# Performance work log

Hardware: AMD Instinct MI355X
Metric: run time of the kernel (lower is better)

Reference implementation:

```python
import jax, jax.numpy as jnp
import numpy as np

B, N, HD = 4, 16384, 1024
H, M = 8, 32
D = HD // H  # 128


def setup_inputs() -> dict:
    key = jax.random.key(0)
    ks = jax.random.split(key, 8)
    std = 0.02
    x = jax.random.normal(ks[0], (B, N, HD), dtype=jnp.float32)
    wt_kv_weight = jax.random.normal(ks[1], (2 * HD, HD), dtype=jnp.float32) * std
    wt_kv_bias = jnp.zeros((2 * HD,), dtype=jnp.float32)
    wtq = jax.random.normal(ks[2], (H, M, D), dtype=jnp.float32) * std
    wtq_bias = jnp.zeros((H, M), dtype=jnp.float32)  # registered buffer, zeros
    qkv_proj = jax.random.normal(ks[3], (H, D, 3 * D), dtype=jnp.float32) * std
    out_weight = jax.random.normal(ks[4], (HD, HD), dtype=jnp.float32) * std
    out_bias = jnp.zeros((HD,), dtype=jnp.float32)
    return {
        'x': x,
        'wt_kv_weight': wt_kv_weight,
        'wt_kv_bias': wt_kv_bias,
        'wtq': wtq,
        'wtq_bias': wtq_bias,
        'qkv_proj': qkv_proj,
        'out_weight': out_weight,
        'out_bias': out_bias,
    }


def reference(x, wt_kv_weight, wt_kv_bias, wtq, wtq_bias, qkv_proj, out_weight, out_bias):
    b, n, hd = x.shape
    h, m, d = wtq.shape
    # wt_kv_proj: Linear(hd, 2hd); torch Linear: x @ W.T + b
    kv = x @ wt_kv_weight.T + wt_kv_bias  # [b, n, 2hd]
    xk, xv = jnp.split(kv, 2, axis=-1)
    xk = xk.reshape(b, n, h, d).transpose(0, 2, 1, 3)  # b h n d
    xv = xv.reshape(b, n, h, d).transpose(0, 2, 1, 3)  # b h n d
    # qk_norm=False -> no normalize
    slice_scores = jnp.einsum('hmd,bhnd->bhmn', wtq, xk)
    slice_weights = jax.nn.softmax(slice_scores, axis=-2)  # softmax over slice axis m
    bias = wtq_bias[..., None]  # [h, m, 1]
    slice_token = jnp.einsum('bhmn,bhnd->bhmd', slice_weights, xv)
    slice_norm = jnp.sum(slice_weights, axis=-1, keepdims=True)  # [b,h,m,1]
    slice_token = slice_token / (slice_norm + 1e-5)
    qkv_token = jnp.einsum('bhmd,hde->bhme', slice_token, qkv_proj)  # e = 3d
    q_tok, k_tok, v_tok = jnp.split(qkv_token, 3, axis=-1)
    scale = d ** (-0.5)
    dots = jnp.einsum('bhqd,bhkd->bhqk', q_tok, k_tok) * scale
    attn_weights = jax.nn.softmax(dots, axis=-1)
    out_token = jnp.einsum('bhqk,bhkd->bhqd', attn_weights, v_tok)
    # scatter back via slice weights
    out = jnp.einsum('bhmd,bhmn->bhnd', out_token, slice_weights)
    out = out.transpose(0, 2, 1, 3).reshape(b, n, hd)
    out = out @ out_weight.T + out_bias  # to_out linear (dropout=0)
    temperature = jnp.asarray(1.0, dtype=x.dtype)
    return (out, slice_weights, temperature, bias, attn_weights)
```

## Files before the change

### kernel.cpp

```cpp
#include <hip/hip_runtime.h>
#include <hip/hip_bf16.h>
#include <stdint.h>

#define BB 4
#define NN 16384
#define HDIM 1024
#define HH 8
#define MM 32
#define DD 128

typedef unsigned int u32;
typedef unsigned short u16;
typedef __attribute__((ext_vector_type(8))) short short8;
typedef __attribute__((ext_vector_type(4))) float f32x4;

__device__ __forceinline__ float bf2f(u16 v) {
    union { u32 u; float f; } c; c.u = ((u32)v) << 16; return c.f;
}
__device__ __forceinline__ u16 f2bf(float f) {
    union { float f; u32 u; } c; c.f = f;
    u32 r = c.u + 0x7fffu + ((c.u >> 16) & 1u);
    return (u16)(r >> 16);
}

__device__ __forceinline__ void gload16(const u16* g, u16* l) {
    __builtin_amdgcn_global_load_lds(
        (const __attribute__((address_space(1))) void*)g,
        (__attribute__((address_space(3))) void*)l, 16, 0, 0);
}

#define MFMA16(a, b, c) __builtin_amdgcn_mfma_f32_16x16x32_bf16(a, b, c, 0, 0, 0)

__global__ __launch_bounds__(256) void convert_kernel(const float* __restrict__ x,
                                                      u16* __restrict__ xb, u16* __restrict__ xbT,
                                                      const float* __restrict__ wtq_bias,
                                                      float* __restrict__ out_misc) {
    __shared__ u32 tl[128 * 65];
    const int t = threadIdx.x;
    const int eb = blockIdx.x & 7;
    const int nb = blockIdx.x >> 3;
    const size_t n0 = (size_t)nb * 128;
    const int e0 = eb * 128;

#pragma unroll 4
    for (int i = 0; i < 32; i++) {
        const int idx = t + i * 256;
        const int nl = idx >> 6, e2 = idx & 63;
        const float2 v = *(const float2*)&x[(n0 + nl) * 1024 + e0 + e2 * 2];
        const u32 pk = (u32)f2bf(v.x) | ((u32)f2bf(v.y) << 16);
        ((u32*)xb)[((n0 + nl) * 1024 + e0) / 2 + e2] = pk;
        tl[nl * 65 + e2] = pk;
    }
    __syncthreads();
    const int b = (int)(n0 >> 14);
    const int nloc = (int)(n0 & 16383);
#pragma unroll 4
    for (int i = 0; i < 32; i++) {
        const int idx = t + i * 256;
        const int el = idx >> 6, n2 = idx & 63;
        const u32 w0 = tl[(2 * n2) * 65 + (el >> 1)];
        const u32 w1 = tl[(2 * n2 + 1) * 65 + (el >> 1)];
        const int sh = (el & 1) * 16;
        const u32 o = ((w0 >> sh) & 0xffffu) | (((w1 >> sh) & 0xffffu) << 16);
        ((u32*)xbT)[((size_t)(b * 1024 + e0 + el) * 16384 + nloc + 2 * n2) >> 1] = o;
    }
    if (blockIdx.x == 0) {
        if (t == 0) out_misc[0] = 1.0f;
        if (t < HH * MM) out_misc[1 + t] = wtq_bias[t];
    }
}

__global__ __launch_bounds__(256) void wq_kernel(const float* __restrict__ wtq,
                                                 const float* __restrict__ wkv,
                                                 const float* __restrict__ bkv,
                                                 u16* __restrict__ WQb, float* __restrict__ wqbias,
                                                 u16* __restrict__ wvb) {
    __shared__ float wtql[MM * DD];
    const int ec = blockIdx.x, h = blockIdx.y, t = threadIdx.x;
    for (int i = t; i < MM * DD; i += 256) wtql[i] = wtq[(size_t)h * MM * DD + i];
    __syncthreads();
    const int m = t >> 3;
    const int e = ec * 128 + (t & 7) * 16;
    float acc[16];
#pragma unroll
    for (int j = 0; j < 16; j++) acc[j] = 0.f;
    for (int d = 0; d < DD; d++) {
        const float wv = wtql[m * DD + d];
        const float4* row = (const float4*)(wkv + (size_t)(h * DD + d) * HDIM + e);
#pragma unroll
        for (int j4 = 0; j4 < 4; j4++) {
            float4 v = row[j4];
            acc[j4 * 4 + 0] += wv * v.x; acc[j4 * 4 + 1] += wv * v.y;
            acc[j4 * 4 + 2] += wv * v.z; acc[j4 * 4 + 3] += wv * v.w;
        }
    }
    u32 pk[8];
#pragma unroll
    for (int p = 0; p < 8; p++)
        pk[p] = (u32)f2bf(acc[2 * p]) | ((u32)f2bf(acc[2 * p + 1]) << 16);
    u16* dst = WQb + (size_t)(h * MM + m) * HDIM + e;
#pragma unroll
    for (int p = 0; p < 2; p++) {
        uint4 q4; q4.x = pk[4 * p]; q4.y = pk[4 * p + 1]; q4.z = pk[4 * p + 2]; q4.w = pk[4 * p + 3];
        *(uint4*)&dst[p * 8] = q4;
    }
    if (ec == 0 && t < MM) {
        float s = 0.f;
        for (int d = 0; d < DD; d++) s += wtql[t * DD + d] * bkv[h * DD + d];
        wqbias[h * MM + t] = s;
    }
    {
        const int blk = blockIdx.y * 8 + blockIdx.x;
        const float4* src = (const float4*)(wkv + (size_t)1024 * 1024);
        for (int i = t; i < 4096; i += 256) {
            const int idx4 = blk * 4096 + i;
            float4 v = src[idx4];
            ushort4 o; o.x = f2bf(v.x); o.y = f2bf(v.y); o.z = f2bf(v.z); o.w = f2bf(v.w);
            ((ushort4*)wvb)[idx4] = o;
        }
    }
}

template<int MODE>
__global__ __launch_bounds__(512, 1) void gemm_nt(
        const u16* __restrict__ A, const u16* __restrict__ Bm,
        const float* __restrict__ bias, void* __restrict__ Cout,
        int NCols, int Kd, int ldk, int ntn, int bofs, int bshift,
        long long bstrideB, long long kCstride) {
    __shared__ u16 ldsA[2][2][8192];
    __shared__ u16 ldsB[2][2][8192];
    const int t = threadIdx.x, l = t & 63, w = t >> 6;
    const int wr = w >> 2, wc = w & 3;

    const int nwg = gridDim.x, cpx = nwg >> 3, bid = blockIdx.x;
    const int swz = (nwg >= 8) ? ((bid & 7) * cpx + (bid >> 3)) : bid;
    const int tm = swz / ntn, tn = swz % ntn;
    const int ks = blockIdx.y;
    const u16* Bb = Bm + (size_t)(tm >> bshift) * bstrideB;

    f32x4 acc[8][4];
    const f32x4 zero = {0.f, 0.f, 0.f, 0.f};
#pragma unroll
    for (int mi = 0; mi < 8; mi++)
#pragma unroll
        for (int ni = 0; ni < 4; ni++) acc[mi][ni] = zero;

    const int srow = w * 8 + (l >> 3);
    const int skel = ((l & 7) ^ ((l >> 3) & 7)) * 8;
    const u16* gA = A  + (size_t)(tm * 256 + srow) * ldk + (size_t)ks * Kd + skel;
    const u16* gB = Bb + (size_t)(tn * 256 + srow) * ldk + (size_t)ks * Kd + skel;
    const int ldo = w * 512 + l * 8;

#define STAGE_A(T, H) { const u16* g_ = gA + (size_t)((H) * 128) * ldk + (T) * 64; \
    u16* d_ = &ldsA[(T) & 1][H][ldo]; gload16(g_, d_); gload16(g_ + (size_t)64 * ldk, d_ + 4096); }
#define STAGE_B(T, H) { const u16* g_ = gB + (size_t)((H) * 128) * ldk + (T) * 64; \
    u16* d_ = &ldsB[(T) & 1][H][ldo]; gload16(g_, d_); gload16(g_ + (size_t)64 * ldk, d_ + 4096); }

    const int m16 = l & 15;
    const int ck0 = (((l >> 4) + 0) ^ (l & 7)) << 3;
    const int ck1 = (((l >> 4) + 4) ^ (l & 7)) << 3;
    const int brb = (wc & 1) * 64;
    const int nT = Kd >> 6;

    STAGE_A(0, 0); STAGE_A(0, 1); STAGE_B(0, 0); STAGE_B(0, 1);
    STAGE_B(1, 0); STAGE_B(1, 1);
    asm volatile("s_waitcnt vmcnt(4)" ::: "memory");
    __builtin_amdgcn_s_barrier();

    for (int kt = 0; kt < nT; ++kt) {
        const int sl = kt & 1;
        const u16* lA = ldsA[sl][wr];
        const u16* lB = ldsB[sl][wc >> 1];
        short8 aF[4][2], bF[4][2];

#pragma unroll
        for (int fr = 0; fr < 4; fr++) {
            aF[fr][0] = *(const short8*)&lA[(fr * 16 + m16) * 64 + ck0];
            aF[fr][1] = *(const short8*)&lA[(fr * 16 + m16) * 64 + ck1];
        }
#pragma unroll
        for (int fc = 0; fc < 2; fc++) {
            bF[fc][0] = *(const short8*)&lB[(brb + fc * 16 + m16) * 64 + ck0];
            bF[fc][1] = *(const short8*)&lB[(brb + fc * 16 + m16) * 64 + ck1];
        }
        if (kt + 1 < nT) STAGE_A(kt + 1, 0);
        __builtin_amdgcn_s_barrier();
        asm volatile("s_waitcnt lgkmcnt(0)" ::: "memory");
        __builtin_amdgcn_s_setprio(1);
#pragma unroll
        for (int kk = 0; kk < 2; kk++)
#pragma unroll
            for (int mi = 0; mi < 4; mi++) {
                acc[mi][0] = MFMA16(aF[mi][kk], bF[0][kk], acc[mi][0]);
                acc[mi][1] = MFMA16(aF[mi][kk], bF[1][kk], acc[mi][1]);
            }
        __builtin_amdgcn_s_setprio(0);
        __builtin_amdgcn_s_barrier();

#pragma unroll
        for (int fc = 2; fc < 4; fc++) {
            bF[fc][0] = *(const short8*)&lB[(brb + fc * 16 + m16) * 64 + ck0];
            bF[fc][1] = *(const short8*)&lB[(brb + fc * 16 + m16) * 64 + ck1];
        }
        if (kt + 1 < nT) STAGE_A(kt + 1, 1);
        __builtin_amdgcn_s_barrier();
        asm volatile("s_waitcnt lgkmcnt(0)" ::: "memory");
        __builtin_amdgcn_s_setprio(1);
#pragma unroll
        for (int kk = 0; kk < 2; kk++)
#pragma unroll
            for (int mi = 0; mi < 4; mi++) {
                acc[mi][2] = MFMA16(aF[mi][kk], bF[2][kk], acc[mi][2]);
                acc[mi][3] = MFMA16(aF[mi][kk], bF[3][kk], acc[mi][3]);
            }
        __builtin_amdgcn_s_setprio(0);
        __builtin_amdgcn_s_barrier();

#pragma unroll
        for (int fr = 0; fr < 4; fr++) {
            aF[fr][0] = *(const short8*)&lA[((fr + 4) * 16 + m16) * 64 + ck0];
            aF[fr][1] = *(const short8*)&lA[((fr + 4) * 16 + m16) * 64 + ck1];
        }
        if (kt + 2 < nT) STAGE_B(kt + 2, 0);
        __builtin_amdgcn_s_barrier();
        asm volatile("s_waitcnt lgkmcnt(0)" ::: "memory");
        __builtin_amdgcn_s_setprio(1);
#pragma unroll
        for (int kk = 0; kk < 2; kk++)
#pragma unroll
            for (int mi = 0; mi < 4; mi++) {
                acc[4 + mi][0] = MFMA16(aF[mi][kk], bF[0][kk], acc[4 + mi][0]);
                acc[4 + mi][1] = MFMA16(aF[mi][kk], bF[1][kk], acc[4 + mi][1]);
            }
        __builtin_amdgcn_s_setprio(0);
        __builtin_amdgcn_s_barrier();

        if (kt + 2 < nT) STAGE_B(kt + 2, 1);
        __builtin_amdgcn_s_barrier();
        __builtin_amdgcn_s_setprio(1);
#pragma unroll
        for (int kk = 0; kk < 2; kk++)
#pragma unroll
            for (int mi = 0; mi < 4; mi++) {
                acc[4 + mi][2] = MFMA16(aF[mi][kk], bF[2][kk], acc[4 + mi][2]);
                acc[4 + mi][3] = MFMA16(aF[mi][kk], bF[3][kk], acc[4 + mi][3]);
            }
        __builtin_amdgcn_s_setprio(0);
        if (kt < nT - 1) {
            if (kt + 2 < nT) asm volatile("s_waitcnt vmcnt(4)" ::: "memory");
            else             asm volatile("s_waitcnt vmcnt(0)" ::: "memory");
            __builtin_amdgcn_s_barrier();
        }
    }
#undef STAGE_A
#undef STAGE_B

    const int cr = (l >> 4) * 4;
    const int cc = l & 15;
    if (MODE == 0) {
        float* Cp = (float*)Cout + (size_t)ks * kCstride;
#pragma unroll
        for (int ni = 0; ni < 4; ni++) {
            const int col = tn * 256 + wc * 64 + ni * 16 + cc;
            const float bv = bias ? bias[col] : 0.0f;
#pragma unroll
            for (int mi = 0; mi < 8; mi++) {
                const int row0 = tm * 256 + wr * 128 + mi * 16 + cr;
#pragma unroll
                for (int q = 0; q < 4; q++)
                    Cp[(size_t)(row0 + q) * NCols + col] = acc[mi][ni][q] + bv;
            }
        }
    } else if (MODE == 2) {
        u16* Cp = (u16*)Cout + (size_t)ks * kCstride;
#pragma unroll
        for (int ni = 0; ni < 4; ni++) {
            const int col = tn * 256 + wc * 64 + ni * 16 + cc;
            const float bv = bias ? bias[col] : 0.0f;
#pragma unroll
            for (int mi = 0; mi < 8; mi++) {
                const int row0 = tm * 256 + wr * 128 + mi * 16 + cr;
#pragma unroll
                for (int q = 0; q < 4; q++)
                    Cp[(size_t)(row0 + q) * NCols + col] = f2bf(acc[mi][ni][q] + bv);
            }
        }
    } else {
        const int b = tm >> 6;
        const size_t nbase = (size_t)(tm & 63) * 256 + wr * 128 + cr;
#pragma unroll
        for (int ni = 0; ni < 4; ni++) {
            const int cg = tn * 256 + wc * 64 + ni * 16 + cc;
            const float bv = bias[bofs + cg];
            u16* rowp = (u16*)Cout + (((size_t)(b * NCols + cg)) << 14) + nbase;
#pragma unroll
            for (int mi = 0; mi < 8; mi++) {
                u32 lo = (u32)f2bf(acc[mi][ni][0] + bv) | ((u32)f2bf(acc[mi][ni][1] + bv) << 16);
                u32 hi = (u32)f2bf(acc[mi][ni][2] + bv) | ((u32)f2bf(acc[mi][ni][3] + bv) << 16);
                uint2 pk; pk.x = lo; pk.y = hi;
                *(uint2*)&rowp[mi * 16] = pk;
            }
        }
    }
}

__global__ __launch_bounds__(256, 2) void gemm_small(
        const u16* __restrict__ A, const u16* __restrict__ Bm,
        const float* __restrict__ bias, float* __restrict__ Cout,
        int Ncols, int Kds, int ldk, int ntn, int bshift,
        long long bstrideB, long long kCstride) {
    __shared__ u16 lds_a[128 * 32];
    __shared__ u16 lds_b[128 * 32];
    const int t = threadIdx.x, l = t & 63, w = t >> 6;
    const int wr = w >> 1, wc = w & 1;

    const int nwg = gridDim.x, cpx = nwg >> 3, bid = blockIdx.x;
    const int swz = (nwg >= 8) ? ((bid & 7) * cpx + (bid >> 3)) : bid;
    const int tm = swz / ntn, tn = swz % ntn;
    const int ks = blockIdx.y;
    const u16* Bb = Bm + (size_t)(tm >> bshift) * bstrideB;

    f32x4 acc[4][4];
    const f32x4 zero = {0.f, 0.f, 0.f, 0.f};
#pragma unroll
    for (int mi = 0; mi < 4; mi++)
#pragma unroll
        for (int ni = 0; ni < 4; ni++) acc[mi][ni] = zero;

    const int srow = w * 32 + (l >> 2);
    const int scol = (l & 3) * 8;
    const u16* ga = A  + (size_t)(tm * 128 + srow) * ldk + (size_t)ks * Kds + scol;
    const u16* gb = Bb + (size_t)(tn * 128 + srow) * ldk + (size_t)ks * Kds + scol;
    u16* la = &lds_a[(w * 32) * 32];
    u16* lb = &lds_b[(w * 32) * 32];
    const size_t rstep = (size_t)16 * ldk;

    const int nK = Kds >> 5;
    const int kg = (l >> 4) * 8;
    const int ra = wr * 64 + (l & 15);
    const int rb = wc * 64 + (l & 15);

    for (int kt = 0; kt < nK; kt++) {
        __syncthreads();
        const int ko = kt << 5;
        gload16(ga + ko,         la);
        gload16(ga + ko + rstep, la + 16 * 32);
        gload16(gb + ko,         lb);
        gload16(gb + ko + rstep, lb + 16 * 32);
        __syncthreads();

        short8 af[4], bfr[4];
#pragma unroll
        for (int mi = 0; mi < 4; mi++) af[mi] = *(const short8*)&lds_a[(ra + mi * 16) * 32 + kg];
#pragma unroll
        for (int ni = 0; ni < 4; ni++) bfr[ni] = *(const short8*)&lds_b[(rb + ni * 16) * 32 + kg];
#pragma unroll
        for (int mi = 0; mi < 4; mi++)
#pragma unroll
            for (int ni = 0; ni < 4; ni++)
                acc[mi][ni] = MFMA16(af[mi], bfr[ni], acc[mi][ni]);
    }

    float* Cp = Cout + (size_t)ks * kCstride;
#pragma unroll
    for (int ni = 0; ni < 4; ni++) {
        const int col = tn * 128 + wc * 64 + ni * 16 + (l & 15);
        const float bv = bias ? bias[col] : 0.0f;
#pragma unroll
        for (int mi = 0; mi < 4; mi++) {
            const int row0 = tm * 128 + wr * 64 + mi * 16 + ((l >> 4) << 2);
#pragma unroll
            for (int q = 0; q < 4; q++)
                Cp[(size_t)(row0 + q) * Ncols + col] = acc[mi][ni][q] + bv;
        }
    }
}

__global__ __launch_bounds__(256, 2) void slice_pass(
        const u16* __restrict__ scoresT,
        float* __restrict__ sw_out, u16* __restrict__ wN, u16* __restrict__ wT,
        float* __restrict__ pnorm) {
    __shared__ u16 sc_lds[MM * 256];
    __shared__ u16 w_lin[MM * 256];
    const int t = threadIdx.x, l = t & 63, w = t >> 6;
    const int bh = blockIdx.y, b = bh >> 3, h = bh & 7;
    const int n0 = blockIdx.x * 256;

    {
        const size_t rb = (size_t)(b * 256 + h * MM);
#pragma unroll
        for (int j = 0; j < 4; j++) {
            const int rl = w * 8 + j * 2 + (l >> 5);
            gload16(scoresT + ((rb + rl) << 14) + n0 + (l & 31) * 8,
                    sc_lds + (w * 8 + j * 2) * 256 + l * 8);
        }
    }
    __syncthreads();

    {
        float sv[MM];
#pragma unroll
        for (int m = 0; m < MM; m++) sv[m] = bf2f(sc_lds[m * 256 + t]);
        float mx = sv[0];
#pragma unroll
        for (int m = 1; m < MM; m++) mx = fmaxf(mx, sv[m]);
        float sum = 0.f;
#pragma unroll
        for (int m = 0; m < MM; m++) { sv[m] = __expf(sv[m] - mx); sum += sv[m]; }
        const float inv = 1.f / sum;
        u32 pk[16];
#pragma unroll
        for (int m = 0; m < MM; m++) {
            const float wv = sv[m] * inv;
            const size_t row = (size_t)bh * MM + m;
            sw_out[row * NN + n0 + t] = wv;
            const u16 wb = f2bf(wv);
            w_lin[m * 256 + t] = wb;
            wN[row * NN + n0 + t] = wb;
            if (m & 1) pk[m >> 1] |= ((u32)wb << 16); else pk[m >> 1] = (u32)wb;
        }
        u16* wrow = wT + ((size_t)(b * NN) + n0 + t) * 256 + h * MM;
#pragma unroll
        for (int p = 0; p < 4; p++) {
            uint4 q4; q4.x = pk[4 * p]; q4.y = pk[4 * p + 1]; q4.z = pk[4 * p + 2]; q4.w = pk[4 * p + 3];
            *(uint4*)&wrow[p * 8] = q4;
        }
    }
    __syncthreads();

    {
        const int pm = t >> 3, ps = t & 7;
        float ssum = 0.f;
        for (int j = 0; j < 32; j++) ssum += bf2f(w_lin[pm * 256 + ps * 32 + j]);
        ssum += __shfl_xor(ssum, 1); ssum += __shfl_xor(ssum, 2); ssum += __shfl_xor(ssum, 4);
        if (ps == 0) pnorm[((size_t)bh * 64 + blockIdx.x) * MM + pm] = ssum;
    }
}

__global__ __launch_bounds__(256) void sum_U(const u16* __restrict__ U_part, u16* __restrict__ U2) {
    const int i = blockIdx.x * 256 + threadIdx.x;
    float4 s = make_float4(0.f, 0.f, 0.f, 0.f);
    for (int ks = 0; ks < 16; ks++) {
        const ushort4 v = ((const ushort4*)(U_part + (size_t)ks * 1048576))[i];
        s.x += bf2f(v.x); s.y += bf2f(v.y); s.z += bf2f(v.z); s.w += bf2f(v.w);
    }
    const int r = i >> 8, e4 = i & 255;
    const int b = r >> 8, h = (r >> 5) & 7, m = r & 31;
    const int r2 = h * 128 + b * 32 + m;
    ushort4 o; o.x = f2bf(s.x); o.y = f2bf(s.y); o.z = f2bf(s.z); o.w = f2bf(s.w);
    ((ushort4*)U2)[r2 * 256 + e4] = o;
}

__global__ __launch_bounds__(256) void st_fix(const float* __restrict__ C2,
                                              const float* __restrict__ pnorm,
                                              const float* __restrict__ bkv,
                                              u16* __restrict__ st_red) {
    __shared__ float norm[MM];
    const int bh = blockIdx.x, b = bh >> 3, h = bh & 7, t = threadIdx.x;
    if (t < MM) {
        float s = 0.f;
        for (int g = 0; g < 64; g++) s += pnorm[((size_t)bh * 64 + g) * MM + t];
        norm[t] = s;
    }
    __syncthreads();
#pragma unroll
    for (int i = 0; i < 16; i++) {
        const int idx = t * 16 + i;
        const int m = idx >> 7, d = idx & 127;
        const float nv = norm[m];
        float c = 0.f;
        const size_t off = (size_t)(h * 128 + d) * 128 + b * 32 + m;
#pragma unroll
        for (int ks = 0; ks < 8; ks++) c += C2[(size_t)ks * 131072 + off];
        const float v = (c + bkv[1024 + h * 128 + d] * nv) / (nv + 1e-5f);
        st_red[(size_t)bh * 4096 + idx] = f2bf(v);
    }
}

__global__ __launch_bounds__(256) void qt_kernel(const u16* __restrict__ st_red,
                                                 const float* __restrict__ qkvp,
                                                 float* __restrict__ qt_g) {
    __shared__ u16 st_lds[MM * DD];
    const int es = blockIdx.x, bh = blockIdx.y, h = bh & 7, t = threadIdx.x;
    {
        const uint4* src = (const uint4*)(st_red + (size_t)bh * 4096);
        ((uint4*)st_lds)[t] = src[t];
        ((uint4*)st_lds)[t + 256] = src[t + 256];
    }
    __syncthreads();
    const float* qw = qkvp + (size_t)h * DD * 384;
#pragma unroll
    for (int i = 0; i < 4; i++) {
        const int idx = t + i * 256;
        const int m = idx >> 5, el = idx & 31;
        const int e = es * 32 + el;
        float s = 0.f;
        for (int d = 0; d < DD; d++) s += bf2f(st_lds[m * DD + d]) * qw[d * 384 + e];
        qt_g[((size_t)bh * MM + m) * 384 + e] = s;
    }
}

__global__ void finalize2_kernel(const float* __restrict__ qt_g,
                                 float* __restrict__ attn_out, float* __restrict__ otw) {
    __shared__ float qt[MM * 384];
    __shared__ float dots[MM * MM];
    const int bh = blockIdx.x, t = threadIdx.x;

#pragma unroll
    for (int i = 0; i < 48; i++) qt[t + i * 256] = qt_g[(size_t)bh * 12288 + t + i * 256];
    __syncthreads();
    const float scale = 0.08838834764831845f;
#pragma unroll
    for (int i = 0; i < 4; i++) {
        int idx = t * 4 + i;
        int qi = idx >> 5, kj = idx & 31;
        float s = 0.f;
        for (int d = 0; d < DD; d++) s += qt[qi * 384 + d] * qt[kj * 384 + 128 + d];
        dots[idx] = s * scale;
    }
    __syncthreads();
    if (t < MM) {
        float mx = -1e30f;
        float ex[MM];
#pragma unroll
        for (int j = 0; j < MM; j++) mx = fmaxf(mx, dots[t * MM + j]);
        float sm = 0.f;
#pragma unroll
        for (int j = 0; j < MM; j++) { ex[j] = __expf(dots[t * MM + j] - mx); sm += ex[j]; }
        float inv = 1.f / sm;
#pragma unroll
        for (int j = 0; j < MM; j++) {
            float v = ex[j] * inv;
            dots[t * MM + j] = v;
            attn_out[((size_t)bh * MM + t) * MM + j] = v;
        }
    }
    __syncthreads();
#pragma unroll
    for (int i = 0; i < 16; i++) {
        int e = t + i * 256;
        int m = e >> 7, d = e & 127;
        float s = 0.f;
#pragma unroll
        for (int j = 0; j < MM; j++) s += dots[m * MM + j] * qt[j * 384 + 256 + d];
        otw[(size_t)bh * 4096 + e] = s;
    }
}

__global__ __launch_bounds__(256) void zmat_kernel(const float* __restrict__ otw,
                                                   const float* __restrict__ outw,
                                                   u16* __restrict__ Zt) {
    __shared__ float ot_lds[MM * DD];
    const int bh = blockIdx.y, b = bh >> 3, h = bh & 7;
    const int es = blockIdx.x;
    const int t = threadIdx.x;
    for (int i = t; i < MM * DD; i += 256) ot_lds[i] = otw[(size_t)bh * 4096 + i];
    __syncthreads();
    const int e = es * 128 + (t >> 1);
    const int m0 = (t & 1) * 16;
    const float* ow = outw + (size_t)e * HDIM + h * DD;
    float acc[16];
#pragma unroll
    for (int m = 0; m < 16; m++) acc[m] = 0.f;
    for (int d = 0; d < DD; d += 4) {
        float4 o4 = *(const float4*)&ow[d];
#pragma unroll
        for (int m = 0; m < 16; m++) {
            const float* otr = &ot_lds[(m0 + m) * DD + d];
            acc[m] += o4.x * otr[0] + o4.y * otr[1] + o4.z * otr[2] + o4.w * otr[3];
        }
    }
    u32 pk[8];
#pragma unroll
    for (int p = 0; p < 8; p++)
        pk[p] = (u32)f2bf(acc[2 * p]) | ((u32)f2bf(acc[2 * p + 1]) << 16);
    u16* dst = Zt + ((size_t)b * 1024 + e) * 256 + h * MM + m0;
#pragma unroll
    for (int p = 0; p < 2; p++) {
        uint4 q4; q4.x = pk[4 * p]; q4.y = pk[4 * p + 1]; q4.z = pk[4 * p + 2]; q4.w = pk[4 * p + 3];
        *(uint4*)&dst[p * 8] = q4;
    }
}

extern "C" void kernel_launch(void* const* d_in, const int* in_sizes, int n_in,
                              void* d_out, int out_size, void* d_ws, size_t ws_size,
                              hipStream_t stream) {
    const float* x        = (const float*)d_in[0];
    const float* wkv      = (const float*)d_in[1];
    const float* bkv      = (const float*)d_in[2];
    const float* wtq      = (const float*)d_in[3];
    const float* wtq_bias = (const float*)d_in[4];
    const float* qkvp     = (const float*)d_in[5];
    const float* outw     = (const float*)d_in[6];
    const float* outb     = (const float*)d_in[7];

    float* out  = (float*)d_out;
    float* out0 = out;
    float* out1 = out + 67108864;
    float* out2 = out + 83886080;
    float* out4 = out + 83886337;

    char* ws = (char*)d_ws;
    u16*   xb     = (u16*)(ws);
    u16*   wT     = xb;
    u16*   xbT    = (u16*)(ws + 134217728);
    u16*   wN     = (u16*)(ws + 268435456);
    u16*   scoresT= (u16*)(ws + 301989888);
    u16*   U_part = (u16*)(ws + 335544320);
    u16*   U2     = (u16*)(ws + 402653184);
    float* C2     = (float*)(ws + 404750336);
    u16*   wvb    = (u16*)(ws + 409468928);
    u16*   WQb    = (u16*)(ws + 411566080);
    float* wqbias = (float*)(ws + 412090368);
    float* pnorm  = (float*)(ws + 412091392);
    u16*   st_red = (u16*)(ws + 412353536);
    float* otws   = (float*)(ws + 412615680);
    u16*   Zt     = (u16*)(ws + 413138944);
    float* qt_g   = (float*)(ws + 415236096);

    convert_kernel<<<dim3(4096), dim3(256), 0, stream>>>(x, xb, xbT, wtq_bias, out2);
    wq_kernel<<<dim3(8, 8), dim3(256), 0, stream>>>(wtq, wkv, bkv, WQb, wqbias, wvb);
    gemm_nt<1><<<dim3(256), dim3(512), 0, stream>>>(xb, WQb, wqbias, (void*)scoresT,
                                                    256, 1024, 1024, 1, 0, 30, 0, 0);
    slice_pass<<<dim3(64, 32), dim3(256), 0, stream>>>(scoresT, out1, wN, wT, pnorm);
    gemm_nt<2><<<dim3(16, 16), dim3(512), 0, stream>>>(wN, xbT, nullptr, (void*)U_part,
                                                       1024, 1024, 16384, 4, 0, 0,
                                                       (long long)16777216, (long long)1048576);
    sum_U<<<dim3(1024), dim3(256), 0, stream>>>(U_part, U2);
    gemm_small<<<dim3(8, 8), dim3(256), 0, stream>>>(wvb, U2, nullptr, C2,
                                                     128, 128, 1024, 1, 0,
                                                     (long long)131072, (long long)131072);
    st_fix<<<dim3(32), dim3(256), 0, stream>>>(C2, pnorm, bkv, st_red);
    qt_kernel<<<dim3(12, 32), dim3(256), 0, stream>>>(st_red, qkvp, qt_g);
    finalize2_kernel<<<dim3(32), dim3(256), 0, stream>>>(qt_g, out4, otws);
    zmat_kernel<<<dim3(8, 32), dim3(256), 0, stream>>>(otws, outw, Zt);
    gemm_small<<<dim3(4096), dim3(256), 0, stream>>>(wT, Zt, outb, out0,
                                                     1024, 256, 256, 8, 7,
                                                     (long long)262144, 0);
}
```

Measured before the change: 527.9 us.

## Fuse slice-score GEMM with softmax, weight writes and norm partials

Result: faster. 505.2 us (-4.3%).

```diff
diff --git a/kernel.cpp b/kernel.cpp
--- a/kernel.cpp
+++ b/kernel.cpp
@@ -121,6 +121,208 @@
     }
 }
 
+__global__ __launch_bounds__(512, 1) void gemm_score_sm(
+        const u16* __restrict__ A, const u16* __restrict__ Bm,
+        const float* __restrict__ bias,
+        float* __restrict__ sw_out, u16* __restrict__ wN, u16* __restrict__ wT,
+        float* __restrict__ pnorm) {
+    __shared__ u16 smem[65536];
+    const int t = threadIdx.x, l = t & 63, w = t >> 6;
+    const int wr = w >> 2, wc = w & 3;
+
+    const int nwg = gridDim.x, cpx = nwg >> 3, bid = blockIdx.x;
+    const int tm = (bid & 7) * cpx + (bid >> 3);
+
+    f32x4 acc[8][4];
+    const f32x4 zero = {0.f, 0.f, 0.f, 0.f};
+#pragma unroll
+    for (int mi = 0; mi < 8; mi++)
+#pragma unroll
+        for (int ni = 0; ni < 4; ni++) acc[mi][ni] = zero;
+
+    const int srow = w * 8 + (l >> 3);
+    const int skel = ((l & 7) ^ ((l >> 3) & 7)) * 8;
+    const u16* gA = A  + (size_t)(tm * 256 + srow) * 1024 + skel;
+    const u16* gB = Bm + (size_t)srow * 1024 + skel;
+    const int ldo = w * 512 + l * 8;
+
+#define LAp(SL, H) (&smem[(SL) * 16384 + (H) * 8192])
+#define LBp(SL, H) (&smem[32768 + (SL) * 16384 + (H) * 8192])
+#define STAGE_A(T, H) { const u16* g_ = gA + (size_t)((H) * 128) * 1024 + (T) * 64; \
+    u16* d_ = LAp((T) & 1, H) + ldo; gload16(g_, d_); gload16(g_ + (size_t)64 * 1024, d_ + 4096); }
+#define STAGE_B(T, H) { const u16* g_ = gB + (size_t)((H) * 128) * 1024 + (T) * 64; \
+    u16* d_ = LBp((T) & 1, H) + ldo; gload16(g_, d_); gload16(g_ + (size_t)64 * 1024, d_ + 4096); }
+
+    const int m16 = l & 15;
+    const int ck0 = (((l >> 4) + 0) ^ (l & 7)) << 3;
+    const int ck1 = (((l >> 4) + 4) ^ (l & 7)) << 3;
+    const int brb = (wc & 1) * 64;
+    const int nT = 16;
+
+    STAGE_A(0, 0); STAGE_A(0, 1); STAGE_B(0, 0); STAGE_B(0, 1);
+    STAGE_B(1, 0); STAGE_B(1, 1);
+    asm volatile("s_waitcnt vmcnt(4)" ::: "memory");
+    __builtin_amdgcn_s_barrier();
+
+    for (int kt = 0; kt < nT; ++kt) {
+        const int sl = kt & 1;
+        const u16* lA = LAp(sl, wr);
+        const u16* lB = LBp(sl, wc >> 1);
+        short8 aF[4][2], bF[4][2];
+
+#pragma unroll
+        for (int fr = 0; fr < 4; fr++) {
+            aF[fr][0] = *(const short8*)&lA[(fr * 16 + m16) * 64 + ck0];
+            aF[fr][1] = *(const short8*)&lA[(fr * 16 + m16) * 64 + ck1];
+        }
+#pragma unroll
+        for (int fc = 0; fc < 2; fc++) {
+            bF[fc][0] = *(const short8*)&lB[(brb + fc * 16 + m16) * 64 + ck0];
+            bF[fc][1] = *(const short8*)&lB[(brb + fc * 16 + m16) * 64 + ck1];
+        }
+        if (kt + 1 < nT) STAGE_A(kt + 1, 0);
+        __builtin_amdgcn_s_barrier();
+        asm volatile("s_waitcnt lgkmcnt(0)" ::: "memory");
+        __builtin_amdgcn_s_setprio(1);
+#pragma unroll
+        for (int kk = 0; kk < 2; kk++)
+#pragma unroll
+            for (int mi = 0; mi < 4; mi++) {
+                acc[mi][0] = MFMA16(aF[mi][kk], bF[0][kk], acc[mi][0]);
+                acc[mi][1] = MFMA16(aF[mi][kk], bF[1][kk], acc[mi][1]);
+            }
+        __builtin_amdgcn_s_setprio(0);
+        __builtin_amdgcn_s_barrier();
+
+#pragma unroll
+        for (int fc = 2; fc < 4; fc++) {
+            bF[fc][0] = *(const short8*)&lB[(brb + fc * 16 + m16) * 64 + ck0];
+            bF[fc][1] = *(const short8*)&lB[(brb + fc * 16 + m16) * 64 + ck1];
+        }
+        if (kt + 1 < nT) STAGE_A(kt + 1, 1);
+        __builtin_amdgcn_s_barrier();
+        asm volatile("s_waitcnt lgkmcnt(0)" ::: "memory");
+        __builtin_amdgcn_s_setprio(1);
+#pragma unroll
+        for (int kk = 0; kk < 2; kk++)
+#pragma unroll
+            for (int mi = 0; mi < 4; mi++) {
+                acc[mi][2] = MFMA16(aF[mi][kk], bF[2][kk], acc[mi][2]);
+                acc[mi][3] = MFMA16(aF[mi][kk], bF[3][kk], acc[mi][3]);
+            }
+        __builtin_amdgcn_s_setprio(0);
+        __builtin_amdgcn_s_barrier();
+
+#pragma unroll
+        for (int fr = 0; fr < 4; fr++) {
+            aF[fr][0] = *(const short8*)&lA[((fr + 4) * 16 + m16) * 64 + ck0];
+            aF[fr][1] = *(const short8*)&lA[((fr + 4) * 16 + m16) * 64 + ck1];
+        }
+        if (kt + 2 < nT) STAGE_B(kt + 2, 0);
+        __builtin_amdgcn_s_barrier();
+        asm volatile("s_waitcnt lgkmcnt(0)" ::: "memory");
+        __builtin_amdgcn_s_setprio(1);
+#pragma unroll
+        for (int kk = 0; kk < 2; kk++)
+#pragma unroll
+            for (int mi = 0; mi < 4; mi++) {
+                acc[4 + mi][0] = MFMA16(aF[mi][kk], bF[0][kk], acc[4 + mi][0]);
+                acc[4 + mi][1] = MFMA16(aF[mi][kk], bF[1][kk], acc[4 + mi][1]);
+            }
+        __builtin_amdgcn_s_setprio(0);
+        __builtin_amdgcn_s_barrier();
+
+        if (kt + 2 < nT) STAGE_B(kt + 2, 1);
+        __builtin_amdgcn_s_barrier();
+        __builtin_amdgcn_s_setprio(1);
+#pragma unroll
+        for (int kk = 0; kk < 2; kk++)
+#pragma unroll
+            for (int mi = 0; mi < 4; mi++) {
+                acc[4 + mi][2] = MFMA16(aF[mi][kk], bF[2][kk], acc[4 + mi][2]);
+                acc[4 + mi][3] = MFMA16(aF[mi][kk], bF[3][kk], acc[4 + mi][3]);
+            }
+        __builtin_amdgcn_s_setprio(0);
+        if (kt < nT - 1) {
+            if (kt + 2 < nT) asm volatile("s_waitcnt vmcnt(4)" ::: "memory");
+            else             asm volatile("s_waitcnt vmcnt(0)" ::: "memory");
+            __builtin_amdgcn_s_barrier();
+        }
+    }
+#undef STAGE_A
+#undef STAGE_B
+#undef LAp
+#undef LBp
+
+    __syncthreads();
+    const int cr = (l >> 4) * 4;
+    const int cc = l & 15;
+#pragma unroll
+    for (int ni = 0; ni < 4; ni++) {
+        const int hm = wc * 64 + ni * 16 + cc;
+        const float bv = bias[hm];
+#pragma unroll
+        for (int mi = 0; mi < 8; mi++) {
+            const int nb_ = wr * 128 + mi * 16 + cr;
+            u32 lo = (u32)f2bf(acc[mi][ni][0] + bv) | ((u32)f2bf(acc[mi][ni][1] + bv) << 16);
+            u32 hi = (u32)f2bf(acc[mi][ni][2] + bv) | ((u32)f2bf(acc[mi][ni][3] + bv) << 16);
+            uint2 pk; pk.x = lo; pk.y = hi;
+            *(uint2*)&smem[hm * 256 + (((nb_ >> 2) ^ (hm & 63)) << 2)] = pk;
+        }
+    }
+    __syncthreads();
+
+    const int b = tm >> 6, g = tm & 63;
+    const int n_ = t & 255, hs = (t >> 8) * 4;
+    const size_t gn = (size_t)g * 256 + n_;
+    for (int h = hs; h < hs + 4; h++) {
+        float sv[MM];
+#pragma unroll
+        for (int m = 0; m < MM; m++) {
+            const int hm = h * 32 + m;
+            sv[m] = bf2f(smem[hm * 256 + (((n_ >> 2) ^ (hm & 63)) << 2) + (n_ & 3)]);
+        }
+        float mx = sv[0];
+#pragma unroll
+        for (int m = 1; m < MM; m++) mx = fmaxf(mx, sv[m]);
+        float sum = 0.f;
+#pragma unroll
+        for (int m = 0; m < MM; m++) { sv[m] = __expf(sv[m] - mx); sum += sv[m]; }
+        const float inv = 1.f / sum;
+        u32 wpk[16];
+#pragma unroll
+        for (int m = 0; m < MM; m++) {
+            const float wv = sv[m] * inv;
+            const int hm = h * 32 + m;
+            const size_t row = (size_t)(b * 256 + hm);
+            sw_out[row * NN + gn] = wv;
+            const u16 wb = f2bf(wv);
+            wN[row * NN + gn] = wb;
+            smem[hm * 256 + (((n_ >> 2) ^ (hm & 63)) << 2) + (n_ & 3)] = wb;
+            if (m & 1) wpk[m >> 1] |= ((u32)wb << 16); else wpk[m >> 1] = (u32)wb;
+        }
+        u16* wrow = wT + ((size_t)(b * NN) + gn) * 256 + h * 32;
+#pragma unroll
+        for (int p = 0; p < 4; p++) {
+            uint4 q4; q4.x = wpk[4 * p]; q4.y = wpk[4 * p + 1]; q4.z = wpk[4 * p + 2]; q4.w = wpk[4 * p + 3];
+            *(uint4*)&wrow[p * 8] = q4;
+        }
+    }
+    __syncthreads();
+
+    {
+        const int hm2 = t >> 1, half = t & 1;
+        float s = 0.f;
+        for (int j = 0; j < 128; j++) {
+            const int n2 = half * 128 + j;
+            s += bf2f(smem[hm2 * 256 + (((n2 >> 2) ^ (hm2 & 63)) << 2) + (n2 & 3)]);
+        }
+        s += __shfl_xor(s, 1);
+        if (half == 0)
+            pnorm[((size_t)(b * 8 + (hm2 >> 5)) * 64 + g) * MM + (hm2 & 31)] = s;
+    }
+}
+
 template<int MODE>
 __global__ __launch_bounds__(512, 1) void gemm_nt(
         const u16* __restrict__ A, const u16* __restrict__ Bm,
@@ -257,8 +459,8 @@
 
     const int cr = (l >> 4) * 4;
     const int cc = l & 15;
-    if (MODE == 0) {
-        float* Cp = (float*)Cout + (size_t)ks * kCstride;
+    if (MODE == 2) {
+        u16* Cp = (u16*)Cout + (size_t)ks * kCstride;
 #pragma unroll
         for (int ni = 0; ni < 4; ni++) {
             const int col = tn * 256 + wc * 64 + ni * 16 + cc;
@@ -268,11 +470,11 @@
                 const int row0 = tm * 256 + wr * 128 + mi * 16 + cr;
 #pragma unroll
                 for (int q = 0; q < 4; q++)
-                    Cp[(size_t)(row0 + q) * NCols + col] = acc[mi][ni][q] + bv;
-            }
-        }
-    } else if (MODE == 2) {
-        u16* Cp = (u16*)Cout + (size_t)ks * kCstride;
+                    Cp[(size_t)(row0 + q) * NCols + col] = f2bf(acc[mi][ni][q] + bv);
+            }
+        }
+    } else {
+        float* Cp = (float*)Cout + (size_t)ks * kCstride;
 #pragma unroll
         for (int ni = 0; ni < 4; ni++) {
             const int col = tn * 256 + wc * 64 + ni * 16 + cc;
@@ -282,23 +484,7 @@
                 const int row0 = tm * 256 + wr * 128 + mi * 16 + cr;
 #pragma unroll
                 for (int q = 0; q < 4; q++)
-                    Cp[(size_t)(row0 + q) * NCols + col] = f2bf(acc[mi][ni][q] + bv);
-            }
-        }
-    } else {
-        const int b = tm >> 6;
-        const size_t nbase = (size_t)(tm & 63) * 256 + wr * 128 + cr;
-#pragma unroll
-        for (int ni = 0; ni < 4; ni++) {
-            const int cg = tn * 256 + wc * 64 + ni * 16 + cc;
-            const float bv = bias[bofs + cg];
-            u16* rowp = (u16*)Cout + (((size_t)(b * NCols + cg)) << 14) + nbase;
-#pragma unroll
-            for (int mi = 0; mi < 8; mi++) {
-                u32 lo = (u32)f2bf(acc[mi][ni][0] + bv) | ((u32)f2bf(acc[mi][ni][1] + bv) << 16);
-                u32 hi = (u32)f2bf(acc[mi][ni][2] + bv) | ((u32)f2bf(acc[mi][ni][3] + bv) << 16);
-                uint2 pk; pk.x = lo; pk.y = hi;
-                *(uint2*)&rowp[mi * 16] = pk;
+                    Cp[(size_t)(row0 + q) * NCols + col] = acc[mi][ni][q] + bv;
             }
         }
     }
@@ -373,67 +559,6 @@
             for (int q = 0; q < 4; q++)
                 Cp[(size_t)(row0 + q) * Ncols + col] = acc[mi][ni][q] + bv;
         }
-    }
-}
-
-__global__ __launch_bounds__(256, 2) void slice_pass(
-        const u16* __restrict__ scoresT,
-        float* __restrict__ sw_out, u16* __restrict__ wN, u16* __restrict__ wT,
-        float* __restrict__ pnorm) {
-    __shared__ u16 sc_lds[MM * 256];
-    __shared__ u16 w_lin[MM * 256];
-    const int t = threadIdx.x, l = t & 63, w = t >> 6;
-    const int bh = blockIdx.y, b = bh >> 3, h = bh & 7;
-    const int n0 = blockIdx.x * 256;
-
-    {
-        const size_t rb = (size_t)(b * 256 + h * MM);
-#pragma unroll
-        for (int j = 0; j < 4; j++) {
-            const int rl = w * 8 + j * 2 + (l >> 5);
-            gload16(scoresT + ((rb + rl) << 14) + n0 + (l & 31) * 8,
-                    sc_lds + (w * 8 + j * 2) * 256 + l * 8);
-        }
-    }
-    __syncthreads();
-
-    {
-        float sv[MM];
-#pragma unroll
-        for (int m = 0; m < MM; m++) sv[m] = bf2f(sc_lds[m * 256 + t]);
-        float mx = sv[0];
-#pragma unroll
-        for (int m = 1; m < MM; m++) mx = fmaxf(mx, sv[m]);
-        float sum = 0.f;
-#pragma unroll
-        for (int m = 0; m < MM; m++) { sv[m] = __expf(sv[m] - mx); sum += sv[m]; }
-        const float inv = 1.f / sum;
-        u32 pk[16];
-#pragma unroll
-        for (int m = 0; m < MM; m++) {
-            const float wv = sv[m] * inv;
-            const size_t row = (size_t)bh * MM + m;
-            sw_out[row * NN + n0 + t] = wv;
-            const u16 wb = f2bf(wv);
-            w_lin[m * 256 + t] = wb;
-            wN[row * NN + n0 + t] = wb;
-            if (m & 1) pk[m >> 1] |= ((u32)wb << 16); else pk[m >> 1] = (u32)wb;
-        }
-        u16* wrow = wT + ((size_t)(b * NN) + n0 + t) * 256 + h * MM;
-#pragma unroll
-        for (int p = 0; p < 4; p++) {
-            uint4 q4; q4.x = pk[4 * p]; q4.y = pk[4 * p + 1]; q4.z = pk[4 * p + 2]; q4.w = pk[4 * p + 3];
-            *(uint4*)&wrow[p * 8] = q4;
-        }
-    }
-    __syncthreads();
-
-    {
-        const int pm = t >> 3, ps = t & 7;
-        float ssum = 0.f;
-        for (int j = 0; j < 32; j++) ssum += bf2f(w_lin[pm * 256 + ps * 32 + j]);
-        ssum += __shfl_xor(ssum, 1); ssum += __shfl_xor(ssum, 2); ssum += __shfl_xor(ssum, 4);
-        if (ps == 0) pnorm[((size_t)bh * 64 + blockIdx.x) * MM + pm] = ssum;
     }
 }
 
@@ -602,10 +727,9 @@
 
     char* ws = (char*)d_ws;
     u16*   xb     = (u16*)(ws);
-    u16*   wT     = xb;
     u16*   xbT    = (u16*)(ws + 134217728);
     u16*   wN     = (u16*)(ws + 268435456);
-    u16*   scoresT= (u16*)(ws + 301989888);
+    u16*   wT     = (u16*)(ws + 301989888);
     u16*   U_part = (u16*)(ws + 335544320);
     u16*   U2     = (u16*)(ws + 402653184);
     float* C2     = (float*)(ws + 404750336);
@@ -620,9 +744,7 @@
 
     convert_kernel<<<dim3(4096), dim3(256), 0, stream>>>(x, xb, xbT, wtq_bias, out2);
     wq_kernel<<<dim3(8, 8), dim3(256), 0, stream>>>(wtq, wkv, bkv, WQb, wqbias, wvb);
-    gemm_nt<1><<<dim3(256), dim3(512), 0, stream>>>(xb, WQb, wqbias, (void*)scoresT,
-                                                    256, 1024, 1024, 1, 0, 30, 0, 0);
-    slice_pass<<<dim3(64, 32), dim3(256), 0, stream>>>(scoresT, out1, wN, wT, pnorm);
+    gemm_score_sm<<<dim3(256), dim3(512), 0, stream>>>(xb, WQb, wqbias, out1, wN, wT, pnorm);
     gemm_nt<2><<<dim3(16, 16), dim3(512), 0, stream>>>(wN, xbT, nullptr, (void*)U_part,
                                                        1024, 1024, 16384, 4, 0, 0,
                                                        (long long)16777216, (long long)1048576);
```
